# Kernel optimization log

Measured on AMD Instinct MI355X. Metric: run time of the kernel, lower is better.

Reference implementation:

```python
import jax, jax.numpy as jnp
import numpy as np

B, L, N, FA, FB, D, OUT, R, T = 128, 128, 6, 39, 10, 200, 1, 3, 2
MB = 256  # num bonds per molecule
NEG = -9e8


def setup_inputs():
    key = jax.random.key(0)
    ks = iter(jax.random.split(key, 64))
    def rn(shape, sc=0.05):
        return jax.random.normal(next(ks), shape, dtype=jnp.float32) * sc
    inp = {}
    inp['atom_list'] = jax.random.normal(next(ks), (B, L, FA), dtype=jnp.float32)
    inp['bond_list'] = jax.random.normal(next(ks), (B, MB, FB), dtype=jnp.float32)
    inp['atom_degree_list'] = jax.random.randint(next(ks), (B, L, N), 0, L, dtype=jnp.int32)
    inp['bond_degree_list'] = jax.random.randint(next(ks), (B, L, N), 0, MB, dtype=jnp.int32)
    inp['atom_mask'] = jnp.ones((B, L), dtype=jnp.float32)
    # parameters (torch Linear: y = x @ W + b with W stored here as [in, out])
    inp['W_atom'] = rn((FA, D)); inp['b_atom'] = rn((D,))
    inp['W_nei'] = rn((FA + FB, D)); inp['b_nei'] = rn((D,))
    inp['W_align'] = rn((R, 2 * D, 1)); inp['b_align'] = rn((R, 1))
    inp['W_attend'] = rn((R, D, D)); inp['b_attend'] = rn((R, D))
    # GRUCell weights, torch layout [3D, D], gate order r,z,n
    inp['Wih'] = rn((R, 3 * D, D)); inp['Whh'] = rn((R, 3 * D, D))
    inp['bih'] = rn((R, 3 * D)); inp['bhh'] = rn((R, 3 * D))
    inp['W_mol_align'] = rn((2 * D, 1)); inp['b_mol_align'] = rn((1,))
    inp['W_mol_attend'] = rn((D, D)); inp['b_mol_attend'] = rn((D,))
    inp['mWih'] = rn((3 * D, D)); inp['mWhh'] = rn((3 * D, D))
    inp['mbih'] = rn((3 * D,)); inp['mbhh'] = rn((3 * D,))
    inp['W_metric'] = rn((2 * D, D)); inp['b_metric'] = rn((D,))
    inp['W_out'] = rn((D, OUT)); inp['b_out'] = rn((OUT,))
    return inp


def _gather(feat, idx):
    # feat [B, M, F], idx [B, L, N] -> [B, L, N, F]
    b, l, n = idx.shape
    g = jnp.take_along_axis(feat, idx.reshape(b, l * n)[..., None], axis=1)
    return g.reshape(b, l, n, feat.shape[-1])


def _gru(x, h, Wih, Whh, bih, bhh):
    gi = x @ Wih.T + bih
    gh = h @ Whh.T + bhh
    ir, iz, inn = jnp.split(gi, 3, axis=-1)
    hr, hz, hn = jnp.split(gh, 3, axis=-1)
    r = jax.nn.sigmoid(ir + hr)
    z = jax.nn.sigmoid(iz + hz)
    n = jnp.tanh(inn + r * hn)
    return (1.0 - z) * n + z * h


def reference(atom_list, bond_list, atom_degree_list, bond_degree_list, atom_mask,
              W_atom, b_atom, W_nei, b_nei, W_align, b_align, W_attend, b_attend,
              Wih, Whh, bih, bhh, W_mol_align, b_mol_align, W_mol_attend, b_mol_attend,
              mWih, mWhh, mbih, mbhh, W_metric, b_metric, W_out, b_out):
    lrelu = jax.nn.leaky_relu
    b, l, _ = atom_list.shape
    atom_feature = lrelu(atom_list @ W_atom + b_atom)          # [B,L,D]
    atom_nei = _gather(atom_list, atom_degree_list)            # [B,L,N,FA]
    bond_nei = _gather(bond_list, bond_degree_list)            # [B,L,N,FB]
    nei = lrelu(jnp.concatenate([atom_nei, bond_nei], -1) @ W_nei + b_nei)  # [B,L,N,D]

    pad = (atom_degree_list == l - 1)
    attend_mask = (~pad).astype(jnp.float32)[..., None]        # [B,L,N,1]
    softmax_mask = jnp.where(pad, NEG, 0.0)[..., None]         # [B,L,N,1]

    h = atom_feature
    cur = atom_feature
    for r in range(R):
        if r > 0:
            nei = _gather(cur, atom_degree_list)
        exp = jnp.broadcast_to(cur[:, :, None, :], nei.shape)
        align = lrelu(jnp.concatenate([exp, nei], -1) @ W_align[r] + b_align[r])
        w = jax.nn.softmax(align + softmax_mask, axis=-2) * attend_mask
        trans = nei @ W_attend[r] + b_attend[r]
        ctx = jax.nn.elu(jnp.sum(w * trans, axis=-2))          # [B,L,D]
        h = _gru(ctx.reshape(-1, D), h.reshape(-1, D), Wih[r], Whh[r], bih[r], bhh[r]).reshape(b, l, D)
        cur = jax.nn.relu(h)

    am = atom_mask[..., None]                                   # [B,L,1]
    mol_feature = jnp.sum(cur * am, axis=-2)                    # [B,D]
    act_mol = jax.nn.relu(mol_feature)
    mol_softmax_mask = jnp.where(am == 0.0, NEG, 0.0)           # [B,L,1]
    for _ in range(T):
        exp = jnp.broadcast_to(act_mol[:, None, :], cur.shape)
        score = lrelu(jnp.concatenate([exp, cur], -1) @ W_mol_align + b_mol_align)
        w = jax.nn.softmax(score + mol_softmax_mask, axis=-2) * am
        trans = cur @ W_mol_attend + b_mol_attend
        ctx = jax.nn.elu(jnp.sum(w * trans, axis=-2))           # [B,D]
        mol_feature = _gru(ctx, mol_feature, mWih, mWhh, mbih, mbhh)
        act_mol = jax.nn.relu(mol_feature)

    dd = jnp.float32(R - 2)  # leaked python loop var `d` in the original
    feat = jnp.concatenate([mol_feature, mol_feature + dd], -1)
    return (feat @ W_metric + b_metric) @ W_out + b_out


if __name__ == '__main__':
    out = reference(**setup_inputs())
    print(out.shape)
```

## Files before the change

### kernel.cpp

```cpp
#include <hip/hip_runtime.h>
#include <hip/hip_bf16.h>
#include <math.h>
#include <string.h>

#define B_ 128
#define L_ 128
#define N_ 6
#define FA_ 39
#define FB_ 10
#define D_ 200
#define MB_ 256
#define R_ 3
#define T_ 2
#define NEGV -9e8f
#define BL_ (B_*L_)
#define G3D_ (3*D_)
#define FP32TAG 0x3F800000u
#define KP 416
#define NP 896
#define KC 224
#define NC 256

typedef __hip_bfloat16 bf16;
typedef __attribute__((ext_vector_type(8))) short short8;
typedef __attribute__((ext_vector_type(4))) float f32x4;

__device__ __forceinline__ float b2f(const bf16 x){ return __bfloat162float(x); }
__device__ __forceinline__ unsigned short f2b(float v){ bf16 t = __float2bfloat16(v); return *reinterpret_cast<unsigned short*>(&t); }
__device__ __forceinline__ float bu2f(unsigned short u){ unsigned x = ((unsigned)u)<<16; float f; memcpy(&f,&x,4); return f; }
__device__ __forceinline__ float lo2f(unsigned x){ unsigned y = x<<16; float f; memcpy(&f,&y,4); return f; }
__device__ __forceinline__ float hi2f(unsigned x){ unsigned y = x & 0xffff0000u; float f; memcpy(&f,&y,4); return f; }
__device__ __forceinline__ float lreluf(float x){ return x>=0.f ? x : 0.01f*x; }
__device__ __forceinline__ float eluf(float x){ return x>0.f ? x : expm1f(x); }
__device__ __forceinline__ float sigmf(float x){ return 1.f/(1.f+expf(-x)); }

#define NSEG 14
struct CvtArgs { const void* src[NSEG]; int ofs[NSEG+1]; };

#define PREPB_N (R_*NP*KP)
#define PREPW_N (R_*NC*KC)
#define PREPM_N (D_*G3D_)
#define PREPG_N (2*PREPM_N)
#define PREPT_N 40000
#define PREPE_N 80000
#define CONV_N 23989
#define XHPAD_N (BL_*16)
#define AROWS (BL_ + B_*MB_)
#define A_N (AROWS*64)
#define BI_N (448*64)

struct PrepArgs {
    CvtArgs cvt;
    const void *Wih, *Whh, *Watt, *mWih, *mWhh, *Wmt, *Wme;
    const void *bond, *Wnei, *atom, *Watom;
    float* conv;
    unsigned short *B2t, *WatT, *WGi, *WGh, *WmtT, *WmeT, *XH, *A16, *Bi16;
    const unsigned* amtag;
    int ew_total;
};

__device__ __forceinline__ float ldd(const void* p, size_t i, bool f32){
    return f32 ? ((const float*)p)[i] : b2f(((const bf16*)p)[i]);
}

__global__ void __launch_bounds__(256) k_prep(PrepArgs A){
    bool f32 = (*A.amtag == FP32TAG);
    int i = blockIdx.x*256 + (int)threadIdx.x;
    if (i >= A.ew_total) return;
    if (i < CONV_N){
        int s = 0;
        while (i >= A.cvt.ofs[s+1]) s++;
        A.conv[i] = ldd(A.cvt.src[s], i - A.cvt.ofs[s], f32);
        return;
    }
    int i2 = i - CONV_N;
    if (i2 < PREPB_N){
        int kk = i2 % KP;
        int rest = i2 / KP;
        int n = rest % NP;
        int r = rest / NP;
        float v = 0.f;
        if (kk < 200){
            if (n < 600) v = ldd(A.Wih, ((size_t)(r*G3D_ + n))*D_ + kk, f32);
        } else if (kk < 400){
            int j = -1;
            if (n < 400) j = n;
            else if (n >= 600 && n < 800) j = n - 200;
            if (j >= 0) v = ldd(A.Whh, ((size_t)(r*G3D_ + j))*D_ + (kk-200), f32);
        }
        A.B2t[i2] = f2b(v);
        return;
    }
    int i3 = i2 - PREPB_N;
    if (i3 < PREPW_N){
        int kk = i3 % KC;
        int rest = i3 / KC;
        int n = rest % NC;
        int r = rest / NC;
        float v = 0.f;
        if (kk < 200 && n < 200) v = ldd(A.Watt, ((size_t)r*D_ + kk)*D_ + n, f32);
        A.WatT[i3] = f2b(v);
        return;
    }
    int i4 = i3 - PREPW_N;
    if (i4 < PREPG_N){
        int half = i4 / PREPM_N;
        int s = i4 - half*PREPM_N;
        (half ? A.WGh : A.WGi)[s] = f2b(ldd(half ? A.mWhh : A.mWih, s, f32));
        return;
    }
    int i5 = i4 - PREPG_N;
    if (i5 < PREPT_N){
        int k = i5 / 200, d = i5 % 200;
        A.WmtT[(size_t)d*200 + k] = f2b(ldd(A.Wmt, i5, f32));
        return;
    }
    int i6 = i5 - PREPT_N;
    if (i6 < PREPE_N){
        int k = i6 / 200, d = i6 % 200;
        A.WmeT[(size_t)d*400 + k] = f2b(ldd(A.Wme, i6, f32));
        return;
    }
    int i7 = i6 - PREPE_N;
    if (i7 < XHPAD_N){
        int al = i7 >> 4, j = i7 & 15;
        A.XH[(size_t)al*KP + 400 + j] = 0;
        return;
    }
    int i8 = i7 - XHPAD_N;
    if (i8 < A_N){
        int row = i8 >> 6, k = i8 & 63;
        float v = 0.f;
        if (row < BL_){
            if (k < FA_) v = ldd(A.atom, (size_t)row*FA_ + k, f32);
        } else {
            int rb = row - BL_;
            if (k >= FA_ && k < FA_+FB_) v = ldd(A.bond, (size_t)rb*FB_ + (k-FA_), f32);
        }
        A.A16[i8] = f2b(v);
        return;
    }
    int i9 = i8 - A_N;
    if (i9 < BI_N){
        int n = i9 >> 6, k = i9 & 63;
        float v = 0.f;
        if (n < 200){
            if (k < FA_) v = ldd(A.Watom, (size_t)k*D_ + n, f32);
        } else if (n < 400){
            if (k < FA_+FB_) v = ldd(A.Wnei, (size_t)k*D_ + (n-200), f32);
        }
        A.Bi16[i9] = f2b(v);
    }
}

__global__ void __launch_bounds__(256) k_initmm(const unsigned short* __restrict__ A16,
        const unsigned short* __restrict__ Bi16,
        const void* __restrict__ batom, const void* __restrict__ bnei,
        unsigned short* __restrict__ XH, unsigned short* __restrict__ P16,
        unsigned short* __restrict__ Q16, const unsigned* __restrict__ amtag){
    __shared__ unsigned short As[128][40];
    __shared__ unsigned short Bs[64][40];
    bool f32 = (*amtag == FP32TAG);
    int tid = threadIdx.x;
    int mt = (int)blockIdx.x / 7, nt = (int)blockIdx.x % 7;
    int m0 = mt*128, n0 = nt*64;
    if (m0 >= BL_ && n0 + 64 <= 200) return;
    int lane = tid & 63, wv = tid >> 6;
    int quad = lane >> 4, lm = lane & 15;
    f32x4 acc[2][4];
    #pragma unroll
    for (int a=0;a<2;a++)
        #pragma unroll
        for (int b=0;b<4;b++) acc[a][b] = (f32x4){0.f,0.f,0.f,0.f};
    for (int ks = 0; ks < 2; ks++){
        int r0_ = tid >> 2, c0 = (tid & 3) * 8;
        int r1_ = (tid + 256) >> 2, c1 = ((tid + 256) & 3) * 8;
        uint4 a0 = *(const uint4*)&A16[(size_t)(m0 + r0_)*64 + ks*32 + c0];
        uint4 a1 = *(const uint4*)&A16[(size_t)(m0 + r1_)*64 + ks*32 + c1];
        uint4 b0 = *(const uint4*)&Bi16[(size_t)(n0 + (tid >> 2))*64 + ks*32 + (tid & 3)*8];
        __syncthreads();
        *(uint4*)&As[r0_][c0] = a0;
        *(uint4*)&As[r1_][c1] = a1;
        *(uint4*)&Bs[tid >> 2][(tid & 3)*8] = b0;
        __syncthreads();
        short8 av0 = *(const short8*)&As[wv*32 + lm][quad*8];
        short8 av1 = *(const short8*)&As[wv*32 + 16 + lm][quad*8];
        #pragma unroll
        for (int ns=0; ns<4; ns++){
            short8 bv = *(const short8*)&Bs[ns*16 + lm][quad*8];
            acc[0][ns] = __builtin_amdgcn_mfma_f32_16x16x32_bf16(av0, bv, acc[0][ns], 0,0,0);
            acc[1][ns] = __builtin_amdgcn_mfma_f32_16x16x32_bf16(av1, bv, acc[1][ns], 0,0,0);
        }
    }
    #pragma unroll
    for (int ms=0; ms<2; ms++)
      #pragma unroll
      for (int ns=0; ns<4; ns++){
        int n = n0 + ns*16 + lm;
        #pragma unroll
        for (int i=0;i<4;i++){
            int row = m0 + wv*32 + ms*16 + quad*4 + i;
            float v = acc[ms][ns][i];
            if (row < BL_){
                if (n < 200){
                    XH[(size_t)row*KP + 200 + n] = f2b(lreluf(v + ldd(batom, n, f32)));
                } else if (n < 400){
                    P16[(size_t)row*D_ + (n-200)] = f2b(v + ldd(bnei, n-200, f32));
                }
            } else if (n >= 200 && n < 400){
                Q16[(size_t)(row-BL_)*D_ + (n-200)] = f2b(v);
            }
        }
      }
}

__global__ void __launch_bounds__(256) k_attn(
        const unsigned short* __restrict__ cur16, const unsigned short* __restrict__ XH,
        const float* __restrict__ s1, const float* __restrict__ tb,
        const int* __restrict__ adl, const int* __restrict__ bdl,
        const unsigned short* __restrict__ P16, const unsigned short* __restrict__ Q16,
        const float* __restrict__ W_align, const float* __restrict__ b_align, int r,
        unsigned short* __restrict__ wnei, float* __restrict__ wsum){
    int bid = blockIdx.x;
    int mol = bid & (B_-1), chunk = bid >> 7;
    int wv = threadIdx.x >> 6, lane = threadIdx.x & 63;
    int al = mol*L_ + chunk*4 + wv;
    __shared__ float s_nei[4][N_][D_];

    int idxn[N_]; bool pad[N_];
    #pragma unroll
    for (int n=0;n<N_;n++){ idxn[n] = adl[al*N_ + n]; pad[n] = (idxn[n] == L_-1); }

    float s2[N_];
    float s1v;
    if (r == 0){
        const float* Wab = W_align + D_;
        float acc[N_+1];
        #pragma unroll
        for (int n=0;n<N_+1;n++) acc[n] = 0.f;
        #pragma unroll
        for (int n=0;n<N_;n++){
            int bd = bdl[al*N_ + n];
            const unsigned short* Prow = P16 + ((size_t)mol*L_ + idxn[n])*D_;
            const unsigned short* Qrow = Q16 + ((size_t)mol*MB_ + bd)*D_;
            for (int d=lane; d<D_; d+=64){
                float v = lreluf(bu2f(Prow[d]) + bu2f(Qrow[d]));
                s_nei[wv][n][d] = v;
                acc[n] += v * Wab[d];
            }
        }
        for (int d=lane; d<D_; d+=64)
            acc[N_] += bu2f(XH[(size_t)al*KP + 200 + d]) * W_align[d];
        #pragma unroll
        for (int o=32;o>0;o>>=1)
            #pragma unroll
            for (int n=0;n<N_+1;n++) acc[n] += __shfl_xor(acc[n],o);
        #pragma unroll
        for (int n=0;n<N_;n++) s2[n] = acc[n];
        s1v = acc[N_];
    } else {
        float tmp = 0.f;
        if (lane < N_) tmp = tb[mol*L_ + idxn[lane]];
        #pragma unroll
        for (int n=0;n<N_;n++) s2[n] = __shfl(tmp, n);
        s1v = s1[al];
    }

    float bav = b_align[r];
    float a[N_]; float mx = -1e30f;
    #pragma unroll
    for (int n=0;n<N_;n++){
        float v = lreluf(s1v + s2[n] + bav);
        if (pad[n]) v += NEGV;
        a[n] = v; mx = fmaxf(mx, v);
    }
    float w[N_]; float se = 0.f;
    #pragma unroll
    for (int n=0;n<N_;n++){ float e = expf(a[n]-mx); w[n]=e; se += e; }
    float inv = 1.f/se; float wsv = 0.f;
    #pragma unroll
    for (int n=0;n<N_;n++){ w[n] = pad[n] ? 0.f : w[n]*inv; wsv += w[n]; }

    if (r == 0){
        for (int d=lane; d<D_; d+=64){
            float acc = 0.f;
            #pragma unroll
            for (int n=0;n<N_;n++) acc += w[n] * s_nei[wv][n][d];
            wnei[(size_t)al*KC + d] = f2b(acc);
        }
    } else {
        for (int d=lane; d<D_; d+=64){
            float acc = 0.f;
            #pragma unroll
            for (int n=0;n<N_;n++) acc += w[n] * bu2f(cur16[((size_t)mol*L_ + idxn[n])*KC + d]);
            wnei[(size_t)al*KC + d] = f2b(acc);
        }
    }
    if (lane < 24) wnei[(size_t)al*KC + 200 + lane] = 0;
    if (lane==0) wsum[al] = wsv;
}

__global__ void __launch_bounds__(256) k_ctxmfma(const unsigned short* __restrict__ Wn,
        const float* __restrict__ wsum, const unsigned short* __restrict__ WatT,
        const float* __restrict__ bias, int r, unsigned short* __restrict__ XH){
    __shared__ unsigned short As[128][40];
    __shared__ unsigned short Bs[64][40];
    int tid = threadIdx.x;
    int m0 = ((int)blockIdx.x & 127) * 128;
    int n0 = ((int)blockIdx.x >> 7) * 64;
    const unsigned short* Bt = WatT + (size_t)r*NC*KC;
    int lane = tid & 63, wv = tid >> 6;
    int quad = lane >> 4, lm = lane & 15;
    f32x4 acc[2][4];
    #pragma unroll
    for (int a=0;a<2;a++)
        #pragma unroll
        for (int b=0;b<4;b++) acc[a][b] = (f32x4){0.f,0.f,0.f,0.f};
    for (int ks = 0; ks < 7; ks++){
        int r0_ = tid >> 2, c0 = (tid & 3) * 8;
        int r1_ = (tid + 256) >> 2, c1 = ((tid + 256) & 3) * 8;
        uint4 a0 = *(const uint4*)&Wn[(size_t)(m0 + r0_)*KC + ks*32 + c0];
        uint4 a1 = *(const uint4*)&Wn[(size_t)(m0 + r1_)*KC + ks*32 + c1];
        uint4 b0 = *(const uint4*)&Bt[(size_t)(n0 + (tid >> 2))*KC + ks*32 + (tid & 3)*8];
        __syncthreads();
        *(uint4*)&As[r0_][c0] = a0;
        *(uint4*)&As[r1_][c1] = a1;
        *(uint4*)&Bs[tid >> 2][(tid & 3)*8] = b0;
        __syncthreads();
        short8 av0 = *(const short8*)&As[wv*32 + lm][quad*8];
        short8 av1 = *(const short8*)&As[wv*32 + 16 + lm][quad*8];
        #pragma unroll
        for (int ns=0; ns<4; ns++){
            short8 bv = *(const short8*)&Bs[ns*16 + lm][quad*8];
            acc[0][ns] = __builtin_amdgcn_mfma_f32_16x16x32_bf16(av0, bv, acc[0][ns], 0,0,0);
            acc[1][ns] = __builtin_amdgcn_mfma_f32_16x16x32_bf16(av1, bv, acc[1][ns], 0,0,0);
        }
    }
    #pragma unroll
    for (int ms=0; ms<2; ms++)
      #pragma unroll
      for (int ns=0; ns<4; ns++){
        int n = n0 + ns*16 + lm;
        if (n < 200){
            float bv = bias[r*D_ + n];
            #pragma unroll
            for (int i=0;i<4;i++){
                int row = m0 + wv*32 + ms*16 + quad*4 + i;
                float v = acc[ms][ns][i] + wsum[row]*bv;
                XH[(size_t)row*KP + n] = f2b(eluf(v));
            }
        }
      }
}

__global__ void __launch_bounds__(256) k_gemm(const unsigned short* __restrict__ XH,
        const unsigned short* __restrict__ B2t, unsigned short* __restrict__ C, int r){
    __shared__ unsigned short As[128][40];
    __shared__ unsigned short Bs[128][40];
    int tid = threadIdx.x;
    int m0 = ((int)blockIdx.x & 127) * 128;
    int n0 = ((int)blockIdx.x >> 7) * 128;
    const unsigned short* Bt = B2t + (size_t)r*NP*KP;
    int lane = tid & 63, wv = tid >> 6;
    int quad = lane >> 4, lm = lane & 15;
    f32x4 acc[2][8];
    #pragma unroll
    for (int a=0;a<2;a++)
        #pragma unroll
        for (int b=0;b<8;b++) acc[a][b] = (f32x4){0.f,0.f,0.f,0.f};
    for (int ks = 0; ks < 13; ks++){
        int r0_ = tid >> 2, c0 = (tid & 3) * 8;
        int r1_ = (tid + 256) >> 2, c1 = ((tid + 256) & 3) * 8;
        uint4 a0 = *(const uint4*)&XH[(size_t)(m0 + r0_)*KP + ks*32 + c0];
        uint4 a1 = *(const uint4*)&XH[(size_t)(m0 + r1_)*KP + ks*32 + c1];
        uint4 b0 = *(const uint4*)&Bt[(size_t)(n0 + r0_)*KP + ks*32 + c0];
        uint4 b1 = *(const uint4*)&Bt[(size_t)(n0 + r1_)*KP + ks*32 + c1];
        __syncthreads();
        *(uint4*)&As[r0_][c0] = a0;
        *(uint4*)&As[r1_][c1] = a1;
        *(uint4*)&Bs[r0_][c0] = b0;
        *(uint4*)&Bs[r1_][c1] = b1;
        __syncthreads();
        short8 av0 = *(const short8*)&As[wv*32 + lm][quad*8];
        short8 av1 = *(const short8*)&As[wv*32 + 16 + lm][quad*8];
        #pragma unroll
        for (int ns=0; ns<8; ns++){
            short8 bv = *(const short8*)&Bs[ns*16 + lm][quad*8];
            acc[0][ns] = __builtin_amdgcn_mfma_f32_16x16x32_bf16(av0, bv, acc[0][ns], 0,0,0);
            acc[1][ns] = __builtin_amdgcn_mfma_f32_16x16x32_bf16(av1, bv, acc[1][ns], 0,0,0);
        }
    }
    #pragma unroll
    for (int ms=0; ms<2; ms++)
      #pragma unroll
      for (int ns=0; ns<8; ns++)
        #pragma unroll
        for (int i=0;i<4;i++){
            int row = m0 + wv*32 + ms*16 + quad*4 + i;
            C[(size_t)row*NP + n0 + ns*16 + lm] = f2b(acc[ms][ns][i]);
        }
}

__global__ void __launch_bounds__(256) k_gru2(const unsigned short* __restrict__ C,
        unsigned short* __restrict__ XH, unsigned short* __restrict__ cur16,
        const float* __restrict__ bih, const float* __restrict__ bhh,
        const float* __restrict__ W_align, const float* __restrict__ Wma, int r,
        float* __restrict__ s1, float* __restrict__ tb, float* __restrict__ curdot){
    int wv = threadIdx.x >> 6, lane = threadIdx.x & 63;
    int al = blockIdx.x*4 + wv;
    size_t base = (size_t)al*NP;
    const float* bi = bih + r*G3D_;
    const float* bh = bhh + r*G3D_;
    const float* Wa = W_align + (r+1)*2*D_;
    bool last = (r == R_-1);
    float a1 = 0.f, a2 = 0.f;
    for (int j = lane; j < D_; j += 64){
        float rsum = bu2f(C[base + j]);
        float zsum = bu2f(C[base + 200 + j]);
        float gin  = bu2f(C[base + 400 + j]);
        float ghn  = bu2f(C[base + 600 + j]);
        float rr = sigmf(rsum + bi[j] + bh[j]);
        float zz = sigmf(zsum + bi[D_+j] + bh[D_+j]);
        float nn = tanhf(gin + bi[2*D_+j] + rr*(ghn + bh[2*D_+j]));
        size_t hx = (size_t)al*KP + 200 + j;
        float hv = bu2f(XH[hx]);
        float hn = (1.f-zz)*nn + zz*hv;
        XH[hx] = f2b(hn);
        float cv = fmaxf(hn, 0.f);
        cur16[(size_t)al*KC + j] = f2b(cv);
        if (last){
            a1 += cv * Wma[D_+j];
        } else {
            a1 += cv * Wa[j];
            a2 += cv * Wa[D_+j];
        }
    }
    if (lane < 24) cur16[(size_t)al*KC + 200 + lane] = 0;
    for (int o=32;o>0;o>>=1){ a1 += __shfl_xor(a1,o); a2 += __shfl_xor(a2,o); }
    if (lane==0){
        if (last) curdot[al] = a1;
        else { s1[al] = a1; tb[al] = a2; }
    }
}

__device__ __forceinline__ float brSum(float v, float* s_red){
    for (int o=32;o>0;o>>=1) v += __shfl_xor(v,o);
    int lane = threadIdx.x & 63, wid = threadIdx.x >> 6;
    __syncthreads();
    if (lane==0) s_red[wid] = v;
    __syncthreads();
    float r = 0.f;
    int nw = blockDim.x >> 6;
    for (int i=0;i<nw;i++) r += s_red[i];
    return r;
}

__device__ __forceinline__ float dot200(const unsigned short* __restrict__ wrow,
                                        const float* __restrict__ v){
    const uint4* wp = (const uint4*)wrow;
    float a0=0.f, a1=0.f;
    #pragma unroll
    for (int kk=0; kk<25; kk++){
        uint4 u = wp[kk];
        f32x4 A = *(const f32x4*)&v[8*kk];
        f32x4 Bv = *(const f32x4*)&v[8*kk+4];
        a0 += A[0]*lo2f(u.x) + A[1]*hi2f(u.x);
        a1 += A[2]*lo2f(u.y) + A[3]*hi2f(u.y);
        a0 += Bv[0]*lo2f(u.z) + Bv[1]*hi2f(u.z);
        a1 += Bv[2]*lo2f(u.w) + Bv[3]*hi2f(u.w);
    }
    return a0 + a1;
}

__global__ void __launch_bounds__(512, 1) k_mol(const unsigned short* __restrict__ cur16,
    const float* __restrict__ curdot, const float* __restrict__ atom_mask,
    const float* __restrict__ Wma, const float* __restrict__ bma,
    const unsigned short* __restrict__ WmtT, const float* __restrict__ bmt,
    const unsigned short* __restrict__ WGi, const unsigned short* __restrict__ WGh,
    const float* __restrict__ mbih, const float* __restrict__ mbhh,
    const unsigned short* __restrict__ WmeT, const float* __restrict__ bme,
    const float* __restrict__ Wout, const float* __restrict__ bout,
    void* __restrict__ out, const unsigned* __restrict__ amtag){
    int b = blockIdx.x, tid = threadIdx.x;
    int wv = tid >> 6, lane = tid & 63;
    int dq = tid & 255, cq = tid >> 8;
    __shared__ unsigned short s_cur[L_*KC];
    __shared__ float s_am[L_], s_neg[L_], s_cd[L_];
    __shared__ float s_wp[4][L_];
    __shared__ __attribute__((aligned(16))) float s_mf[D_];
    __shared__ __attribute__((aligned(16))) float s_act[D_];
    __shared__ __attribute__((aligned(16))) float s_wc[D_];
    __shared__ __attribute__((aligned(16))) float s_ctx[D_];
    __shared__ __attribute__((aligned(16))) float s_mf2[2*D_];
    __shared__ float s_gi[G3D_], s_gh[G3D_];
    __shared__ float s_wma[D_], s_bmt[D_], s_bi[G3D_], s_bh[G3D_];
    __shared__ float s_part[2][256];
    __shared__ float s_red[8];
    __shared__ float s_wsm;
    const uint4* src = (const uint4*)(cur16 + (size_t)b*L_*KC);
    for (int i = tid; i < L_*KC/8; i += 512) ((uint4*)s_cur)[i] = src[i];
    if (tid < L_){
        float am = atom_mask[b*L_ + tid];
        s_am[tid] = am;
        s_neg[tid] = (am == 0.f) ? NEGV : 0.f;
        s_cd[tid] = curdot[b*L_ + tid];
    }
    if (tid < D_){ s_wma[tid] = Wma[tid]; s_bmt[tid] = bmt[tid]; }
    for (int j = tid; j < G3D_; j += 512){
        s_bi[j] = mbih[j];
        s_bh[j] = mbhh[j];
    }
    __syncthreads();
    {
        float a0 = 0.f, a1 = 0.f;
        if (dq < D_)
            for (int l=cq*64; l<cq*64+64; l+=2){
                a0 += bu2f(s_cur[l*KC + dq]) * s_am[l];
                a1 += bu2f(s_cur[(l+1)*KC + dq]) * s_am[l+1];
            }
        s_part[cq][dq] = a0 + a1;
        __syncthreads();
        if (tid < D_){
            float v = s_part[0][tid] + s_part[1][tid];
            s_mf[tid] = v; s_act[tid] = fmaxf(v, 0.f);
        }
        __syncthreads();
    }
    float bma0 = bma[0];
    #pragma unroll 1
    for (int t=0;t<T_;t++){
        if (wv < 4){
            float a = s_act[lane]*s_wma[lane] + s_act[lane+64]*s_wma[lane+64];
            a += s_act[lane+128]*s_wma[lane+128];
            if (lane < 8) a += s_act[lane+192]*s_wma[lane+192];
            #pragma unroll
            for (int o=32;o>0;o>>=1) a += __shfl_xor(a,o);
            float sc0 = lreluf(a + s_cd[lane] + bma0) + s_neg[lane];
            float sc1 = lreluf(a + s_cd[lane+64] + bma0) + s_neg[lane+64];
            float m = fmaxf(sc0, sc1);
            #pragma unroll
            for (int o=32;o>0;o>>=1) m = fmaxf(m, __shfl_xor(m,o));
            float e0 = expf(sc0 - m), e1 = expf(sc1 - m);
            float s = e0 + e1;
            #pragma unroll
            for (int o=32;o>0;o>>=1) s += __shfl_xor(s,o);
            float inv = 1.f/s;
            float w0 = e0*inv*s_am[lane], w1 = e1*inv*s_am[lane+64];
            float ws = w0 + w1;
            #pragma unroll
            for (int o=32;o>0;o>>=1) ws += __shfl_xor(ws,o);
            s_wp[wv][lane] = w0; s_wp[wv][lane+64] = w1;
            if (tid == 0) s_wsm = ws;
            if (tid < D_){
                float acc = 0.f;
                #pragma unroll 16
                for (int l=0; l<L_; l++)
                    acc += s_wp[wv][l] * bu2f(s_cur[l*KC + tid]);
                s_wc[tid] = acc;
            }
        } else {
            int h = tid - 256;
            #pragma unroll 1
            for (int rr=0; rr<3; rr++){
                int row = h + rr*256;
                if (row < G3D_)
                    s_gh[row] = dot200(WGh + (size_t)row*D_, s_mf);
                __builtin_amdgcn_sched_barrier(0);
            }
        }
        __syncthreads();
        if (tid < D_){
            float acc = dot200(WmtT + (size_t)tid*D_, s_wc);
            s_ctx[tid] = eluf(acc + s_wsm * s_bmt[tid]);
        }
        __syncthreads();
        {
            #pragma unroll 1
            for (int rr=0; rr<2; rr++){
                int row = tid + rr*512;
                if (row < G3D_)
                    s_gi[row] = dot200(WGi + (size_t)row*D_, s_ctx);
                __builtin_amdgcn_sched_barrier(0);
            }
        }
        __syncthreads();
        if (tid < D_){
            int d = tid;
            float rr = sigmf(s_gi[d] + s_bi[d] + s_gh[d] + s_bh[d]);
            float zz = sigmf(s_gi[D_+d] + s_bi[D_+d] + s_gh[D_+d] + s_bh[D_+d]);
            float nn = tanhf(s_gi[2*D_+d] + s_bi[2*D_+d] + rr*(s_gh[2*D_+d] + s_bh[2*D_+d]));
            float nm = (1.f-zz)*nn + zz*s_mf[d];
            s_mf[d] = nm; s_act[d] = fmaxf(nm, 0.f);
        }
        __syncthreads();
        __builtin_amdgcn_sched_barrier(0);
    }
    const float dd = (float)(R_ - 2);
    if (tid < 2*D_) s_mf2[tid] = (tid < D_) ? s_mf[tid] : s_mf[tid - D_] + dd;
    __syncthreads();
    float p2 = 0.f;
    if (tid < D_){
        const uint4* wp = (const uint4*)(WmeT + (size_t)tid*400);
        float a0=0.f, a1=0.f;
        #pragma unroll
        for (int kk=0; kk<50; kk++){
            uint4 u = wp[kk];
            f32x4 wA = *(const f32x4*)&s_mf2[8*kk];
            f32x4 wB = *(const f32x4*)&s_mf2[8*kk+4];
            a0 += wA[0]*lo2f(u.x) + wA[1]*hi2f(u.x);
            a1 += wA[2]*lo2f(u.y) + wA[3]*hi2f(u.y);
            a0 += wB[0]*lo2f(u.z) + wB[1]*hi2f(u.z);
            a1 += wB[2]*lo2f(u.w) + wB[3]*hi2f(u.w);
        }
        p2 = (a0 + a1 + bme[tid]) * Wout[tid];
    }
    float o = brSum(p2, s_red);
    if (tid==0){
        o += bout[0];
        if (*amtag == FP32TAG) ((float*)out)[b] = o;
        else ((bf16*)out)[b] = __float2bfloat16(o);
    }
}

extern "C" void kernel_launch(void* const* d_in, const int* in_sizes, int n_in,
                              void* d_out, int out_size, void* d_ws, size_t ws_size,
                              hipStream_t stream) {
    const int* adl = (const int*)d_in[2];
    const int* bdl = (const int*)d_in[3];
    const unsigned* amtag = (const unsigned*)d_in[4];

    static const int srcidx[NSEG] = {4,9,10,12,15,16,17,18,20,23,24,26,27,28};
    static const int segsz[NSEG]  = {16384,1200,3,600,1800,1800,400,1,200,600,600,200,200,1};
    CvtArgs ca;
    int ofs[NSEG+1]; ofs[0] = 0;
    for (int i=0;i<NSEG;i++){ ca.src[i] = d_in[srcidx[i]]; ca.ofs[i] = ofs[i]; ofs[i+1] = ofs[i] + segsz[i]; }
    ca.ofs[NSEG] = ofs[NSEG];

    float* ws   = (float*)d_ws;
    float* conv = ws;
    unsigned short* XH    = (unsigned short*)(conv + 24000);
    unsigned short* B2t   = XH + (size_t)BL_*KP;
    unsigned short* WatT  = B2t + PREPB_N;
    unsigned short* WGi   = WatT + PREPW_N;
    unsigned short* WGh   = WGi + PREPM_N;
    unsigned short* WmtT  = WGh + PREPM_N;
    unsigned short* WmeT  = WmtT + PREPT_N;
    unsigned short* Bi16  = WmeT + PREPE_N;
    unsigned short* cur16 = Bi16 + BI_N;
    unsigned short* creg  = cur16 + (size_t)BL_*KC;
    unsigned short* C = creg;
    unsigned short* A16  = creg;
    unsigned short* wnei = creg;
    unsigned short* Q16  = creg + (size_t)BL_*KC;
    unsigned short* P16  = Q16 + (size_t)B_*MB_*D_;
    float* s1     = (float*)(creg + (size_t)BL_*NP);
    float* tb     = s1 + BL_;
    float* wsum   = tb + BL_;
    float* curdot = wsum + BL_;

    const float* c_amask = conv + ofs[0];
    const float* c_Walign= conv + ofs[1];
    const float* c_balign= conv + ofs[2];
    const float* c_batt  = conv + ofs[3];
    const float* c_bih   = conv + ofs[4];
    const float* c_bhh   = conv + ofs[5];
    const float* c_Wma   = conv + ofs[6];
    const float* c_bma   = conv + ofs[7];
    const float* c_bmt   = conv + ofs[8];
    const float* c_mbih  = conv + ofs[9];
    const float* c_mbhh  = conv + ofs[10];
    const float* c_bme   = conv + ofs[11];
    const float* c_Wout  = conv + ofs[12];
    const float* c_bout  = conv + ofs[13];

    PrepArgs A;
    A.cvt = ca;
    A.Wih = d_in[13]; A.Whh = d_in[14]; A.Watt = d_in[11];
    A.mWih = d_in[21]; A.mWhh = d_in[22]; A.Wmt = d_in[19]; A.Wme = d_in[25];
    A.bond = d_in[1]; A.Wnei = d_in[7]; A.atom = d_in[0]; A.Watom = d_in[5];
    A.conv = conv;
    A.B2t = B2t; A.WatT = WatT; A.WGi = WGi; A.WGh = WGh; A.WmtT = WmtT; A.WmeT = WmeT;
    A.XH = XH; A.A16 = A16; A.Bi16 = Bi16;
    A.amtag = amtag;
    A.ew_total = CONV_N + PREPB_N + PREPW_N + PREPG_N + PREPT_N + PREPE_N
               + XHPAD_N + A_N + BI_N;

    k_prep<<<(A.ew_total + 255)/256, 256, 0, stream>>>(A);
    k_initmm<<<(AROWS/128)*7, 256, 0, stream>>>(A16, Bi16, d_in[6], d_in[8],
                                                XH, P16, Q16, amtag);

    for (int r=0; r<R_; r++){
        k_attn<<<BL_/4, 256, 0, stream>>>(cur16, XH, s1, tb, adl, bdl, P16, Q16,
                                          c_Walign, c_balign, r, wnei, wsum);
        k_ctxmfma<<<(BL_/128)*(NC/64), 256, 0, stream>>>(wnei, wsum, WatT, c_batt, r, XH);
        k_gemm<<<(BL_/128)*(NP/128), 256, 0, stream>>>(XH, B2t, C, r);
        k_gru2<<<BL_/4, 256, 0, stream>>>(C, XH, cur16, c_bih, c_bhh,
                                          c_Walign, c_Wma, r, s1, tb, curdot);
    }

    k_mol<<<B_, 512, 0, stream>>>(cur16, curdot, c_amask, c_Wma, c_bma, WmtT, c_bmt,
                                  WGi, WGh, c_mbih, c_mbhh, WmeT, c_bme, c_Wout, c_bout,
                                  d_out, amtag);
}
```

Before: 416.4 us.

## Fuse GRU gate GEMM with GRU epilogue using interleaved gate columns

Merges the GRU gate GEMM and the separate GRU elementwise kernel into one kernel. The weight matrix is reordered so each 128-column slice holds the r, z, input-n and hidden-n gates for the same output features, and the GRU update runs directly on the accumulators. This removes the write and re-read of the bf16 gate matrix C and one launch per round. Because a block now reads and writes the hidden state at the same time, the state ping-pongs between two buffers, and the align dot products are reduced with atomics after zeroing in the context kernel. In exchange the fused kernel uses more registers and LDS at 512 threads per block, and the second hidden-state buffer is placed over the Q16 scratch region, which must not still be needed.

```diff
diff --git a/kernel.cpp b/kernel.cpp
--- a/kernel.cpp
+++ b/kernel.cpp
@@ -18,6 +18,7 @@
 #define FP32TAG 0x3F800000u
 #define KP 416
 #define NP 896
+#define NP2 1024
 #define KC 224
 #define NC 256
 
@@ -37,7 +38,7 @@
 #define NSEG 14
 struct CvtArgs { const void* src[NSEG]; int ofs[NSEG+1]; };
 
-#define PREPB_N (R_*NP*KP)
+#define PREPB_N (R_*NP2*KP)
 #define PREPW_N (R_*NC*KC)
 #define PREPM_N (D_*G3D_)
 #define PREPG_N (2*PREPM_N)
@@ -45,6 +46,7 @@
 #define PREPE_N 80000
 #define CONV_N 23989
 #define XHPAD_N (BL_*16)
+#define CPAD_N (BL_*24)
 #define AROWS (BL_ + B_*MB_)
 #define A_N (AROWS*64)
 #define BI_N (448*64)
@@ -54,7 +56,7 @@
     const void *Wih, *Whh, *Watt, *mWih, *mWhh, *Wmt, *Wme;
     const void *bond, *Wnei, *atom, *Watom;
     float* conv;
-    unsigned short *B2t, *WatT, *WGi, *WGh, *WmtT, *WmeT, *XH, *A16, *Bi16;
+    unsigned short *B2t, *WatT, *WGi, *WGh, *WmtT, *WmeT, *XH, *A16, *Bi16, *cur16;
     const unsigned* amtag;
     int ew_total;
 };
@@ -77,16 +79,20 @@
     if (i2 < PREPB_N){
         int kk = i2 % KP;
         int rest = i2 / KP;
-        int n = rest % NP;
-        int r = rest / NP;
+        int c = rest % NP2;
+        int r = rest / NP2;
+        int g = c >> 8, n = c & 255;
         float v = 0.f;
-        if (kk < 200){
-            if (n < 600) v = ldd(A.Wih, ((size_t)(r*G3D_ + n))*D_ + kk, f32);
-        } else if (kk < 400){
-            int j = -1;
-            if (n < 400) j = n;
-            else if (n >= 600 && n < 800) j = n - 200;
-            if (j >= 0) v = ldd(A.Whh, ((size_t)(r*G3D_ + j))*D_ + (kk-200), f32);
+        if (n < 200){
+            if (g <= 1){
+                int j = g*200 + n;
+                if (kk < 200) v = ldd(A.Wih, ((size_t)(r*G3D_ + j))*D_ + kk, f32);
+                else if (kk < 400) v = ldd(A.Whh, ((size_t)(r*G3D_ + j))*D_ + (kk-200), f32);
+            } else if (g == 2){
+                if (kk < 200) v = ldd(A.Wih, ((size_t)(r*G3D_ + 400 + n))*D_ + kk, f32);
+            } else {
+                if (kk >= 200 && kk < 400) v = ldd(A.Whh, ((size_t)(r*G3D_ + 400 + n))*D_ + (kk-200), f32);
+            }
         }
         A.B2t[i2] = f2b(v);
         return;
@@ -127,7 +133,13 @@
         A.XH[(size_t)al*KP + 400 + j] = 0;
         return;
     }
-    int i8 = i7 - XHPAD_N;
+    int i7b = i7 - XHPAD_N;
+    if (i7b < CPAD_N){
+        int al = i7b / 24, j = i7b % 24;
+        A.cur16[(size_t)al*KC + 200 + j] = 0;
+        return;
+    }
+    int i8 = i7b - CPAD_N;
     if (i8 < A_N){
         int row = i8 >> 6, k = i8 & 63;
         float v = 0.f;
@@ -302,12 +314,20 @@
 
 __global__ void __launch_bounds__(256) k_ctxmfma(const unsigned short* __restrict__ Wn,
         const float* __restrict__ wsum, const unsigned short* __restrict__ WatT,
-        const float* __restrict__ bias, int r, unsigned short* __restrict__ XH){
+        const float* __restrict__ bias, int r, unsigned short* __restrict__ XH,
+        float* __restrict__ s1, float* __restrict__ tb, float* __restrict__ curdot){
     __shared__ unsigned short As[128][40];
     __shared__ unsigned short Bs[64][40];
     int tid = threadIdx.x;
     int m0 = ((int)blockIdx.x & 127) * 128;
     int n0 = ((int)blockIdx.x >> 7) * 64;
+    if (n0 == 0 && tid < 128){
+        int row = m0 + tid;
+        s1[row] = 0.f; tb[row] = 0.f;
+        if (r == R_-1) curdot[row] = 0.f;
+        #pragma unroll
+        for (int j=0;j<16;j++) XH[(size_t)row*KP + 400 + j] = 0;
+    }
     const unsigned short* Bt = WatT + (size_t)r*NC*KC;
     int lane = tid & 63, wv = tid >> 6;
     int quad = lane >> 4, lm = lane & 15;
@@ -353,93 +373,114 @@
       }
 }
 
-__global__ void __launch_bounds__(256) k_gemm(const unsigned short* __restrict__ XH,
-        const unsigned short* __restrict__ B2t, unsigned short* __restrict__ C, int r){
+__global__ void __launch_bounds__(512, 1) k_gemm2(
+        const unsigned short* __restrict__ XHr, unsigned short* __restrict__ XHw,
+        const unsigned short* __restrict__ B2t, unsigned short* __restrict__ cur16,
+        const float* __restrict__ bih, const float* __restrict__ bhh,
+        const float* __restrict__ W_align, const float* __restrict__ Wma,
+        float* __restrict__ s1, float* __restrict__ tb, float* __restrict__ curdot,
+        int r){
     __shared__ unsigned short As[128][40];
-    __shared__ unsigned short Bs[128][40];
+    __shared__ unsigned short Bs[512][40];
+    __shared__ float s_ab[4][128][2];
     int tid = threadIdx.x;
     int m0 = ((int)blockIdx.x & 127) * 128;
-    int n0 = ((int)blockIdx.x >> 7) * 128;
-    const unsigned short* Bt = B2t + (size_t)r*NP*KP;
+    int half = (int)blockIdx.x >> 7;
+    const unsigned short* Bt = B2t + (size_t)r*NP2*KP;
     int lane = tid & 63, wv = tid >> 6;
+    int wm = wv >> 2, wn = wv & 3;
     int quad = lane >> 4, lm = lane & 15;
-    f32x4 acc[2][8];
-    #pragma unroll
-    for (int a=0;a<2;a++)
+    f32x4 acc[4][8];
+    #pragma unroll
+    for (int a=0;a<4;a++)
         #pragma unroll
         for (int b=0;b<8;b++) acc[a][b] = (f32x4){0.f,0.f,0.f,0.f};
+    int ar = tid >> 2, ac = (tid & 3) * 8;
     for (int ks = 0; ks < 13; ks++){
-        int r0_ = tid >> 2, c0 = (tid & 3) * 8;
-        int r1_ = (tid + 256) >> 2, c1 = ((tid + 256) & 3) * 8;
-        uint4 a0 = *(const uint4*)&XH[(size_t)(m0 + r0_)*KP + ks*32 + c0];
-        uint4 a1 = *(const uint4*)&XH[(size_t)(m0 + r1_)*KP + ks*32 + c1];
-        uint4 b0 = *(const uint4*)&Bt[(size_t)(n0 + r0_)*KP + ks*32 + c0];
-        uint4 b1 = *(const uint4*)&Bt[(size_t)(n0 + r1_)*KP + ks*32 + c1];
-        __syncthreads();
-        *(uint4*)&As[r0_][c0] = a0;
-        *(uint4*)&As[r1_][c1] = a1;
-        *(uint4*)&Bs[r0_][c0] = b0;
-        *(uint4*)&Bs[r1_][c1] = b1;
-        __syncthreads();
-        short8 av0 = *(const short8*)&As[wv*32 + lm][quad*8];
-        short8 av1 = *(const short8*)&As[wv*32 + 16 + lm][quad*8];
-        #pragma unroll
-        for (int ns=0; ns<8; ns++){
-            short8 bv = *(const short8*)&Bs[ns*16 + lm][quad*8];
-            acc[0][ns] = __builtin_amdgcn_mfma_f32_16x16x32_bf16(av0, bv, acc[0][ns], 0,0,0);
-            acc[1][ns] = __builtin_amdgcn_mfma_f32_16x16x32_bf16(av1, bv, acc[1][ns], 0,0,0);
-        }
-    }
-    #pragma unroll
-    for (int ms=0; ms<2; ms++)
-      #pragma unroll
-      for (int ns=0; ns<8; ns++)
-        #pragma unroll
-        for (int i=0;i<4;i++){
-            int row = m0 + wv*32 + ms*16 + quad*4 + i;
-            C[(size_t)row*NP + n0 + ns*16 + lm] = f2b(acc[ms][ns][i]);
-        }
-}
-
-__global__ void __launch_bounds__(256) k_gru2(const unsigned short* __restrict__ C,
-        unsigned short* __restrict__ XH, unsigned short* __restrict__ cur16,
-        const float* __restrict__ bih, const float* __restrict__ bhh,
-        const float* __restrict__ W_align, const float* __restrict__ Wma, int r,
-        float* __restrict__ s1, float* __restrict__ tb, float* __restrict__ curdot){
-    int wv = threadIdx.x >> 6, lane = threadIdx.x & 63;
-    int al = blockIdx.x*4 + wv;
-    size_t base = (size_t)al*NP;
+        uint4 a0 = *(const uint4*)&XHr[(size_t)(m0 + ar)*KP + ks*32 + ac];
+        uint4 bq[4];
+        #pragma unroll
+        for (int q=0;q<4;q++)
+            bq[q] = *(const uint4*)&Bt[(size_t)(q*256 + half*128 + ar)*KP + ks*32 + ac];
+        __syncthreads();
+        *(uint4*)&As[ar][ac] = a0;
+        #pragma unroll
+        for (int q=0;q<4;q++) *(uint4*)&Bs[ar + 128*q][ac] = bq[q];
+        __syncthreads();
+        short8 av[4];
+        #pragma unroll
+        for (int mm=0;mm<4;mm++) av[mm] = *(const short8*)&As[wm*64 + mm*16 + lm][quad*8];
+        #pragma unroll
+        for (int jp=0; jp<8; jp++){
+            int lf = wn + 4*jp;
+            short8 bv = *(const short8*)&Bs[lf*16 + lm][quad*8];
+            #pragma unroll
+            for (int mm=0;mm<4;mm++)
+                acc[mm][jp] = __builtin_amdgcn_mfma_f32_16x16x32_bf16(av[mm], bv, acc[mm][jp], 0,0,0);
+        }
+    }
+    if (tid < 128){
+        #pragma unroll
+        for (int q=0;q<4;q++){ s_ab[q][tid][0] = 0.f; s_ab[q][tid][1] = 0.f; }
+    }
+    __syncthreads();
     const float* bi = bih + r*G3D_;
     const float* bh = bhh + r*G3D_;
     const float* Wa = W_align + (r+1)*2*D_;
     bool last = (r == R_-1);
-    float a1 = 0.f, a2 = 0.f;
-    for (int j = lane; j < D_; j += 64){
-        float rsum = bu2f(C[base + j]);
-        float zsum = bu2f(C[base + 200 + j]);
-        float gin  = bu2f(C[base + 400 + j]);
-        float ghn  = bu2f(C[base + 600 + j]);
-        float rr = sigmf(rsum + bi[j] + bh[j]);
-        float zz = sigmf(zsum + bi[D_+j] + bh[D_+j]);
-        float nn = tanhf(gin + bi[2*D_+j] + rr*(ghn + bh[2*D_+j]));
-        size_t hx = (size_t)al*KP + 200 + j;
-        float hv = bu2f(XH[hx]);
-        float hn = (1.f-zz)*nn + zz*hv;
-        XH[hx] = f2b(hn);
-        float cv = fmaxf(hn, 0.f);
-        cur16[(size_t)al*KC + j] = f2b(cv);
-        if (last){
-            a1 += cv * Wma[D_+j];
-        } else {
-            a1 += cv * Wa[j];
-            a2 += cv * Wa[D_+j];
-        }
-    }
-    if (lane < 24) cur16[(size_t)al*KC + 200 + lane] = 0;
-    for (int o=32;o>0;o>>=1){ a1 += __shfl_xor(a1,o); a2 += __shfl_xor(a2,o); }
-    if (lane==0){
-        if (last) curdot[al] = a1;
-        else { s1[al] = a1; tb[al] = a2; }
+    #pragma unroll
+    for (int mm=0; mm<4; mm++){
+        float pa[4] = {0.f,0.f,0.f,0.f}, pb[4] = {0.f,0.f,0.f,0.f};
+        #pragma unroll
+        for (int jj=0; jj<2; jj++){
+            int d = half*128 + (wn + 4*jj)*16 + lm;
+            if (d < 200){
+                float bir=bi[d], biz=bi[D_+d], bin=bi[2*D_+d];
+                float bhr=bh[d], bhz=bh[D_+d], bhn=bh[2*D_+d];
+                float wa1 = last ? Wma[D_+d] : Wa[d];
+                float wa2 = last ? 0.f : Wa[D_+d];
+                #pragma unroll
+                for (int i=0;i<4;i++){
+                    int row = m0 + wm*64 + mm*16 + quad*4 + i;
+                    float rsum = acc[mm][0+jj][i];
+                    float zsum = acc[mm][2+jj][i];
+                    float gin  = acc[mm][4+jj][i];
+                    float ghn  = acc[mm][6+jj][i];
+                    float rr = sigmf(rsum + bir + bhr);
+                    float zz = sigmf(zsum + biz + bhz);
+                    float nn = tanhf(gin + bin + rr*(ghn + bhn));
+                    size_t hx = (size_t)row*KP + 200 + d;
+                    float hv = bu2f(XHr[hx]);
+                    float hn = (1.f-zz)*nn + zz*hv;
+                    XHw[hx] = f2b(hn);
+                    float cv = fmaxf(hn, 0.f);
+                    cur16[(size_t)row*KC + d] = f2b(cv);
+                    pa[i] += cv * wa1;
+                    pb[i] += cv * wa2;
+                }
+            }
+        }
+        #pragma unroll
+        for (int o=1;o<16;o<<=1){
+            #pragma unroll
+            for (int i=0;i<4;i++){ pa[i] += __shfl_xor(pa[i],o); pb[i] += __shfl_xor(pb[i],o); }
+        }
+        if (lm == 0){
+            #pragma unroll
+            for (int i=0;i<4;i++){
+                int lr = wm*64 + mm*16 + quad*4 + i;
+                s_ab[wn][lr][0] = pa[i];
+                s_ab[wn][lr][1] = pb[i];
+            }
+        }
+    }
+    __syncthreads();
+    if (tid < 128){
+        int row = m0 + tid;
+        float a1 = (s_ab[0][tid][0] + s_ab[1][tid][0]) + (s_ab[2][tid][0] + s_ab[3][tid][0]);
+        float a2 = (s_ab[0][tid][1] + s_ab[1][tid][1]) + (s_ab[2][tid][1] + s_ab[3][tid][1]);
+        if (last) atomicAdd(&curdot[row], a1);
+        else { atomicAdd(&s1[row], a1); atomicAdd(&tb[row], a2); }
     }
 }
 
@@ -638,8 +679,8 @@
 
     float* ws   = (float*)d_ws;
     float* conv = ws;
-    unsigned short* XH    = (unsigned short*)(conv + 24000);
-    unsigned short* B2t   = XH + (size_t)BL_*KP;
+    unsigned short* XHa   = (unsigned short*)(conv + 24000);
+    unsigned short* B2t   = XHa + (size_t)BL_*KP;
     unsigned short* WatT  = B2t + PREPB_N;
     unsigned short* WGi   = WatT + PREPW_N;
     unsigned short* WGh   = WGi + PREPM_N;
@@ -648,11 +689,11 @@
     unsigned short* Bi16  = WmeT + PREPE_N;
     unsigned short* cur16 = Bi16 + BI_N;
     unsigned short* creg  = cur16 + (size_t)BL_*KC;
-    unsigned short* C = creg;
     unsigned short* A16  = creg;
     unsigned short* wnei = creg;
     unsigned short* Q16  = creg + (size_t)BL_*KC;
     unsigned short* P16  = Q16 + (size_t)B_*MB_*D_;
+    unsigned short* XHb  = Q16;
     float* s1     = (float*)(creg + (size_t)BL_*NP);
     float* tb     = s1 + BL_;
     float* wsum   = tb + BL_;
@@ -680,22 +721,24 @@
     A.bond = d_in[1]; A.Wnei = d_in[7]; A.atom = d_in[0]; A.Watom = d_in[5];
     A.conv = conv;
     A.B2t = B2t; A.WatT = WatT; A.WGi = WGi; A.WGh = WGh; A.WmtT = WmtT; A.WmeT = WmeT;
-    A.XH = XH; A.A16 = A16; A.Bi16 = Bi16;
+    A.XH = XHa; A.A16 = A16; A.Bi16 = Bi16; A.cur16 = cur16;
     A.amtag = amtag;
     A.ew_total = CONV_N + PREPB_N + PREPW_N + PREPG_N + PREPT_N + PREPE_N
-               + XHPAD_N + A_N + BI_N;
+               + XHPAD_N + CPAD_N + A_N + BI_N;
 
     k_prep<<<(A.ew_total + 255)/256, 256, 0, stream>>>(A);
     k_initmm<<<(AROWS/128)*7, 256, 0, stream>>>(A16, Bi16, d_in[6], d_in[8],
-                                                XH, P16, Q16, amtag);
+                                                XHa, P16, Q16, amtag);
 
     for (int r=0; r<R_; r++){
-        k_attn<<<BL_/4, 256, 0, stream>>>(cur16, XH, s1, tb, adl, bdl, P16, Q16,
+        unsigned short* XHr = (r & 1) ? XHb : XHa;
+        unsigned short* XHw = (r & 1) ? XHa : XHb;
+        k_attn<<<BL_/4, 256, 0, stream>>>(cur16, XHa, s1, tb, adl, bdl, P16, Q16,
                                           c_Walign, c_balign, r, wnei, wsum);
-        k_ctxmfma<<<(BL_/128)*(NC/64), 256, 0, stream>>>(wnei, wsum, WatT, c_batt, r, XH);
-        k_gemm<<<(BL_/128)*(NP/128), 256, 0, stream>>>(XH, B2t, C, r);
-        k_gru2<<<BL_/4, 256, 0, stream>>>(C, XH, cur16, c_bih, c_bhh,
-                                          c_Walign, c_Wma, r, s1, tb, curdot);
+        k_ctxmfma<<<(BL_/128)*(NC/64), 256, 0, stream>>>(wnei, wsum, WatT, c_batt, r, XHr,
+                                                         s1, tb, curdot);
+        k_gemm2<<<256, 512, 0, stream>>>(XHr, XHw, B2t, cur16, c_bih, c_bhh,
+                                         c_Walign, c_Wma, s1, tb, curdot, r);
     }
 
     k_mol<<<B_, 512, 0, stream>>>(cur16, curdot, c_amask, c_Wma, c_bma, WmtT, c_bmt,
```

New measurement: 452.1 us. +8.6%, slower.
